# Performance work log

Measured on AMD Instinct MI355X. Metric: run time of the kernel, lower is better.

Reference implementation:

```python
import jax, jax.numpy as jnp
import numpy as np

N, D, H = 24, 256, 8
F = D // H  # 32


def setup_inputs() -> dict:
    key = jax.random.key(0)
    ks = jax.random.split(key, 9)
    T = 8192
    x = jax.random.normal(ks[0], (T, N * D), dtype=jnp.float32)
    s = 0.02
    # Joint-specific query weights: (H, N, D, F); shared K/V: (H, D, F)
    Wq = jax.random.normal(ks[1], (H, N, D, F), dtype=jnp.float32) * s
    bq = jax.random.normal(ks[2], (H, N, F), dtype=jnp.float32) * s
    Wk = jax.random.normal(ks[3], (H, D, F), dtype=jnp.float32) * s
    bk = jax.random.normal(ks[4], (H, F), dtype=jnp.float32) * s
    Wv = jax.random.normal(ks[5], (H, D, F), dtype=jnp.float32) * s
    bv = jax.random.normal(ks[6], (H, F), dtype=jnp.float32) * s
    gamma = jnp.ones((N * D,), dtype=jnp.float32)
    beta = jnp.zeros((N * D,), dtype=jnp.float32)
    return {"x": x, "Wq": Wq, "bq": bq, "Wk": Wk, "bk": bk,
            "Wv": Wv, "bv": bv, "gamma": gamma, "beta": beta}


def reference(x, Wq, bq, Wk, bk, Wv, bv, gamma, beta):
    T = x.shape[0]
    xr = x.reshape(T, N, D)                                   # (T, N, D)
    # Shared K/V per head, joint-specific Q per head
    k = jnp.einsum('tnd,hdf->thnf', xr, Wk) + bk[None, :, None, :]
    v = jnp.einsum('tnd,hdf->thnf', xr, Wv) + bv[None, :, None, :]
    q = jnp.einsum('tnd,hndf->thnf', xr, Wq) + bq[None, :, :, :]
    scores = jnp.einsum('thnf,thmf->thnm', q, k) / jnp.sqrt(jnp.float32(F))
    attn = jax.nn.softmax(scores, axis=-1)                    # (T, H, N, N)
    out = jnp.einsum('thnm,thmf->thnf', attn, v)              # (T, H, N, F)
    # Concat heads -> (T, N, H*F) = (T, N, D)
    out = jnp.transpose(out, (0, 2, 1, 3)).reshape(T, N * D)
    # Dropout is identity in eval mode; residual + LayerNorm over N*D
    y = x + out
    mu = jnp.mean(y, axis=-1, keepdims=True)
    var = jnp.mean((y - mu) ** 2, axis=-1, keepdims=True)
    y = (y - mu) * jax.lax.rsqrt(var + 1e-5)
    return y * gamma + beta
```

## Files before the change

### kernel.cpp

```cpp
#include <hip/hip_runtime.h>

#define NT 8192
#define NJ 24
#define DD 256
#define NH 8
#define FF 32
#define C3 768

typedef __attribute__((ext_vector_type(8))) short bf16x8;
typedef __attribute__((ext_vector_type(4))) float f32x4;

__device__ __forceinline__ unsigned short f2bf(float f) {
    union { float f; unsigned int u; } c; c.f = f;
    unsigned int u = c.u;
    unsigned int r = (u + 0x7fffu + ((u >> 16) & 1u)) >> 16;
    return (unsigned short)r;
}
__device__ __forceinline__ float u2f(unsigned int u) {
    union { unsigned int u; float f; } c; c.u = u;
    return c.f;
}
__device__ __forceinline__ void up8(uint4 w, float* f) {
    f[0] = u2f(w.x << 16); f[1] = u2f(w.x & 0xffff0000u);
    f[2] = u2f(w.y << 16); f[3] = u2f(w.y & 0xffff0000u);
    f[4] = u2f(w.z << 16); f[5] = u2f(w.z & 0xffff0000u);
    f[6] = u2f(w.w << 16); f[7] = u2f(w.w & 0xffff0000u);
}

__device__ __forceinline__ void gload16(const void* g, void* l) {
    __builtin_amdgcn_global_load_lds(
        (const __attribute__((address_space(1))) unsigned int*)g,
        (__attribute__((address_space(3))) unsigned int*)l, 16, 0, 0);
}

__global__ void pack_w(const float* __restrict__ Wq, const float* __restrict__ Wk,
                       const float* __restrict__ Wv, unsigned short* __restrict__ wbt) {
    size_t idx = (size_t)blockIdx.x * 256 + threadIdx.x;
    const size_t total = (size_t)NJ * C3 * DD;
    if (idx >= total) return;
    int d = idx & 255;
    int rest = (int)(idx >> 8);
    int c = rest % C3;
    int n = rest / C3;
    float v;
    if (c < 256) {
        int h = c >> 5, f = c & 31;
        v = Wq[((((size_t)h * NJ + n) * DD) + d) * FF + f];
    } else if (c < 512) {
        int cc = c - 256; int h = cc >> 5, f = cc & 31;
        v = Wk[(((size_t)h * DD) + d) * FF + f];
    } else {
        int cc = c - 512; int h = cc >> 5, f = cc & 31;
        v = Wv[(((size_t)h * DD) + d) * FF + f];
    }
    wbt[idx] = f2bf(v);
}

__global__ void pack_b(const float* __restrict__ bq, const float* __restrict__ bk,
                       const float* __restrict__ bv, float* __restrict__ bias) {
    int idx = blockIdx.x * 256 + threadIdx.x;
    if (idx >= NJ * C3) return;
    int c = idx % C3;
    int n = idx / C3;
    float v;
    if (c < 256) {
        int h = c >> 5, f = c & 31;
        v = bq[((h * NJ + n) * FF) + f];
    } else if (c < 512) {
        int cc = c - 256; int h = cc >> 5, f = cc & 31;
        v = bk[h * FF + f];
    } else {
        int cc = c - 512; int h = cc >> 5, f = cc & 31;
        v = bv[h * FF + f];
    }
    bias[idx] = v;
}

__global__ void pack_x(const float* __restrict__ x, unsigned short* __restrict__ xb) {
    size_t idx = (size_t)blockIdx.x * 256 + threadIdx.x;
    const size_t total = (size_t)NT * NJ * DD / 4;
    if (idx >= total) return;
    float4 v = ((const float4*)x)[idx];
    ushort4 h;
    h.x = f2bf(v.x); h.y = f2bf(v.y); h.z = f2bf(v.z); h.w = f2bf(v.w);
    ((ushort4*)xb)[idx] = h;
}

#define BM 128
#define BN 128

__global__ __launch_bounds__(256, 3)
void gemm_qkv(const unsigned short* __restrict__ xb, const unsigned short* __restrict__ wbt,
              const float* __restrict__ bias, unsigned short* __restrict__ qkv,
              int t0, int mbs) {
    const int nwg = gridDim.x;
    const int cpx = nwg >> 3;
    const int bid = blockIdx.x;
    const int swz = (bid & 7) * cpx + (bid >> 3);
    const int nb = swz % 6;
    const int rest = swz / 6;
    const int mb = rest % mbs;
    const int nj = rest / mbs;

    const int tid = threadIdx.x;
    const int wave = tid >> 6, lane = tid & 63;

    __shared__ unsigned short As[BM * 64];
    __shared__ unsigned short Bs[BN * 64];

    f32x4 acc[4][4];
    #pragma unroll
    for (int i = 0; i < 4; ++i)
        #pragma unroll
        for (int j = 0; j < 4; ++j)
            #pragma unroll
            for (int r = 0; r < 4; ++r) acc[i][j][r] = 0.f;

    const int trow0 = t0 + mb * BM;
    const char* srcA = (const char*)(xb + (size_t)trow0 * (NJ * DD) + nj * DD);
    const char* srcB = (const char*)(wbt + ((size_t)nj * C3 + (size_t)nb * BN) * DD);

    const int rg = lane >> 3;
    const int sc = (lane & 7) ^ rg;

    const int wr = (wave >> 1) * 64;
    const int wc = (wave & 1) * 64;
    const int lr = lane & 15;
    const int g  = lane >> 4;

    for (int kb = 0; kb < 4; ++kb) {
        #pragma unroll
        for (int i = 0; i < 4; ++i) {
            int row0 = wave * 32 + i * 8;
            gload16(srcA + (size_t)(row0 + rg) * (NJ * DD * 2) + kb * 128 + sc * 16,
                    (char*)As + row0 * 128);
        }
        #pragma unroll
        for (int i = 0; i < 4; ++i) {
            int row0 = wave * 32 + i * 8;
            gload16(srcB + (size_t)(row0 + rg) * (DD * 2) + kb * 128 + sc * 16,
                    (char*)Bs + row0 * 128);
        }
        __syncthreads();

        #pragma unroll
        for (int kk = 0; kk < 2; ++kk) {
            bf16x8 a[4], b[4];
            #pragma unroll
            for (int i = 0; i < 4; ++i) {
                int row = wr + i * 16 + lr;
                int c16 = (kk * 4 + g) ^ (row & 7);
                a[i] = *(const bf16x8*)((const char*)As + row * 128 + c16 * 16);
            }
            #pragma unroll
            for (int j = 0; j < 4; ++j) {
                int row = wc + j * 16 + lr;
                int c16 = (kk * 4 + g) ^ (row & 7);
                b[j] = *(const bf16x8*)((const char*)Bs + row * 128 + c16 * 16);
            }
            #pragma unroll
            for (int i = 0; i < 4; ++i)
                #pragma unroll
                for (int j = 0; j < 4; ++j)
                    acc[i][j] = __builtin_amdgcn_mfma_f32_16x16x32_bf16(a[i], b[j], acc[i][j], 0, 0, 0);
        }
        __syncthreads();
    }

    const int ln = lane & 15;
    const int lq = (lane >> 4) * 4;
    float bv[4];
    #pragma unroll
    for (int j = 0; j < 4; ++j)
        bv[j] = bias[nj * C3 + nb * BN + wc + j * 16 + ln];
    #pragma unroll
    for (int i = 0; i < 4; ++i) {
        #pragma unroll
        for (int r = 0; r < 4; ++r) {
            int trow = mb * BM + wr + i * 16 + lq + r;
            size_t base = ((size_t)trow * NJ + nj) * C3 + (size_t)nb * BN;
            #pragma unroll
            for (int j = 0; j < 4; ++j) {
                float val = acc[i][j][r] + bv[j];
                qkv[base + wc + j * 16 + ln] = f2bf(val);
            }
        }
    }
}

__global__ __launch_bounds__(256, 4)
void attn_ln(const unsigned short* __restrict__ qkv, const float* __restrict__ x,
             const float* __restrict__ gamma, const float* __restrict__ beta,
             float* __restrict__ out, int t0) {
    const int tloc = blockIdx.x;
    const int t = t0 + tloc;
    const int tid = threadIdx.x;
    const int wave = tid >> 6, lane = tid & 63;

    __shared__ __align__(16) char smem[NJ * C3 * 2];
    unsigned short* qs = (unsigned short*)smem;
    float* os = (float*)smem;
    __shared__ float red[8];
    __shared__ float stats[2];

    {
        const int4* src = (const int4*)(qkv + (size_t)tloc * NJ * C3);
        int4* dst = (int4*)qs;
        #pragma unroll
        for (int j = 0; j < 9; ++j)
            dst[tid + j * 256] = src[tid + j * 256];
    }
    __syncthreads();

    float o[FF];
    const bool active = tid < NH * NJ;
    int hn = 0, nn = 0;
    if (active) {
        const int h = tid / NJ;
        const int n = tid - h * NJ;
        hn = h; nn = n;
        const int hb = h * FF;
        float qf[FF];
        {
            const uint4* qp = (const uint4*)(qs + n * C3 + hb);
            #pragma unroll
            for (int jj = 0; jj < 4; ++jj) { uint4 w = qp[jj]; up8(w, &qf[jj * 8]); }
        }
        float s[NJ];
        float mx = -1e30f;
        for (int m = 0; m < NJ; ++m) {
            const uint4* kp = (const uint4*)(qs + m * C3 + 256 + hb);
            float a = 0.f;
            #pragma unroll
            for (int jj = 0; jj < 4; ++jj) {
                uint4 w = kp[jj];
                float kf[8]; up8(w, kf);
                #pragma unroll
                for (int e = 0; e < 8; ++e) a += qf[jj * 8 + e] * kf[e];
            }
            a *= 0.17677669529663687f;
            s[m] = a;
            mx = fmaxf(mx, a);
        }
        float sum = 0.f;
        for (int m = 0; m < NJ; ++m) { s[m] = __expf(s[m] - mx); sum += s[m]; }
        float inv = 1.f / sum;
        #pragma unroll
        for (int f = 0; f < FF; ++f) o[f] = 0.f;
        for (int m = 0; m < NJ; ++m) {
            float w = s[m] * inv;
            const uint4* vp = (const uint4*)(qs + m * C3 + 512 + hb);
            #pragma unroll
            for (int jj = 0; jj < 4; ++jj) {
                uint4 wv = vp[jj];
                float vf[8]; up8(wv, vf);
                #pragma unroll
                for (int e = 0; e < 8; ++e) o[jj * 8 + e] += w * vf[e];
            }
        }
    }
    __syncthreads();
    if (active) {
        float* dst = os + nn * DD + hn * FF;
        #pragma unroll
        for (int jj = 0; jj < 8; ++jj)
            *(float4*)(dst + jj * 4) = make_float4(o[jj * 4], o[jj * 4 + 1], o[jj * 4 + 2], o[jj * 4 + 3]);
    }
    __syncthreads();

    const float4* x4 = (const float4*)(x + (size_t)t * (NJ * DD));
    const float4* o4 = (const float4*)os;
    float4 yv[6];
    float sum = 0.f, sq = 0.f;
    #pragma unroll
    for (int j = 0; j < 6; ++j) {
        float4 a = x4[tid + j * 256];
        float4 b = o4[tid + j * 256];
        float4 y;
        y.x = a.x + b.x; y.y = a.y + b.y; y.z = a.z + b.z; y.w = a.w + b.w;
        yv[j] = y;
        sum += y.x + y.y + y.z + y.w;
        sq  += y.x * y.x + y.y * y.y + y.z * y.z + y.w * y.w;
    }
    #pragma unroll
    for (int off = 32; off > 0; off >>= 1) {
        sum += __shfl_down(sum, off);
        sq  += __shfl_down(sq, off);
    }
    if (lane == 0) { red[wave] = sum; red[4 + wave] = sq; }
    __syncthreads();
    if (tid == 0) {
        float s = red[0] + red[1] + red[2] + red[3];
        float q = red[4] + red[5] + red[6] + red[7];
        float mu = s * (1.f / 6144.f);
        float var = q * (1.f / 6144.f) - mu * mu;
        stats[0] = mu;
        stats[1] = rsqrtf(var + 1e-5f);
    }
    __syncthreads();
    const float mu = stats[0], rs = stats[1];
    const float4* g4 = (const float4*)gamma;
    const float4* b4 = (const float4*)beta;
    float4* out4 = (float4*)(out + (size_t)t * (NJ * DD));
    #pragma unroll
    for (int j = 0; j < 6; ++j) {
        float4 g = g4[tid + j * 256];
        float4 bb = b4[tid + j * 256];
        float4 y = yv[j];
        y.x = (y.x - mu) * rs * g.x + bb.x;
        y.y = (y.y - mu) * rs * g.y + bb.y;
        y.z = (y.z - mu) * rs * g.z + bb.z;
        y.w = (y.w - mu) * rs * g.w + bb.w;
        out4[tid + j * 256] = y;
    }
}

extern "C" void kernel_launch(void* const* d_in, const int* in_sizes, int n_in,
                              void* d_out, int out_size, void* d_ws, size_t ws_size,
                              hipStream_t stream) {
    const float* x     = (const float*)d_in[0];
    const float* Wq    = (const float*)d_in[1];
    const float* bq    = (const float*)d_in[2];
    const float* Wk    = (const float*)d_in[3];
    const float* bk    = (const float*)d_in[4];
    const float* Wv    = (const float*)d_in[5];
    const float* bv    = (const float*)d_in[6];
    const float* gamma = (const float*)d_in[7];
    const float* beta  = (const float*)d_in[8];
    float* out = (float*)d_out;

    char* ws = (char*)d_ws;
    const size_t wbt_bytes  = (size_t)NJ * C3 * DD * 2;
    const size_t bias_bytes = (size_t)NJ * C3 * 4;
    const size_t xb_bytes   = (size_t)NT * NJ * DD * 2;
    unsigned short* wbt = (unsigned short*)ws;
    float* bias = (float*)(ws + wbt_bytes);
    unsigned short* xb  = (unsigned short*)(ws + wbt_bytes + bias_bytes);
    unsigned short* qkv = (unsigned short*)(ws + wbt_bytes + bias_bytes + xb_bytes);

    const size_t fixed = wbt_bytes + bias_bytes + xb_bytes;
    size_t avail = (ws_size > fixed) ? ws_size - fixed : 0;
    int chunk = NT;
    while (chunk > BM && (size_t)chunk * NJ * C3 * 2 > avail) chunk >>= 1;

    const size_t wtotal = (size_t)NJ * C3 * DD;
    pack_w<<<dim3((unsigned)((wtotal + 255) / 256)), dim3(256), 0, stream>>>(Wq, Wk, Wv, wbt);
    pack_b<<<dim3((NJ * C3 + 255) / 256), dim3(256), 0, stream>>>(bq, bk, bv, bias);
    const size_t xtotal4 = (size_t)NT * NJ * DD / 4;
    pack_x<<<dim3((unsigned)((xtotal4 + 255) / 256)), dim3(256), 0, stream>>>(x, xb);

    for (int t0 = 0; t0 < NT; t0 += chunk) {
        int mbs = chunk / BM;
        gemm_qkv<<<dim3(6 * mbs * NJ), dim3(256), 0, stream>>>(xb, wbt, bias, qkv, t0, mbs);
        attn_ln<<<dim3(chunk), dim3(256), 0, stream>>>(qkv, x, gamma, beta, out, t0);
    }
}
```

Baseline: 643.4 us.

## Switch QKV to fp16 with packed dot2 attention and slimmer LDS staging

Changes the packed x, weights and QKV intermediate from bf16 to fp16, using the fp16 MFMA in the projection GEMM. In the attention kernel, scores are computed with packed fp16 dot2 instructions and the PV accumulation uses packed half2 FMAs instead of unpacking to fp32. Only K/V are staged in shared memory, with Q read directly from global, and the output tile is XOR-swizzled to reduce LDS bank conflicts. Accumulating the attention output in fp16 reduces precision, and fp16 has a narrower range than bf16.

```diff
diff --git a/kernel.cpp b/kernel.cpp
--- a/kernel.cpp
+++ b/kernel.cpp
@@ -7,24 +7,25 @@
 #define FF 32
 #define C3 768
 
-typedef __attribute__((ext_vector_type(8))) short bf16x8;
+typedef __attribute__((ext_vector_type(8))) _Float16 f16x8;
+typedef __attribute__((ext_vector_type(2))) _Float16 half2v;
 typedef __attribute__((ext_vector_type(4))) float f32x4;
 
-__device__ __forceinline__ unsigned short f2bf(float f) {
-    union { float f; unsigned int u; } c; c.f = f;
-    unsigned int u = c.u;
-    unsigned int r = (u + 0x7fffu + ((u >> 16) & 1u)) >> 16;
-    return (unsigned short)r;
-}
-__device__ __forceinline__ float u2f(unsigned int u) {
-    union { unsigned int u; float f; } c; c.u = u;
-    return c.f;
-}
-__device__ __forceinline__ void up8(uint4 w, float* f) {
-    f[0] = u2f(w.x << 16); f[1] = u2f(w.x & 0xffff0000u);
-    f[2] = u2f(w.y << 16); f[3] = u2f(w.y & 0xffff0000u);
-    f[4] = u2f(w.z << 16); f[5] = u2f(w.z & 0xffff0000u);
-    f[6] = u2f(w.w << 16); f[7] = u2f(w.w & 0xffff0000u);
+__device__ __forceinline__ unsigned short f2h(float f) {
+    union { _Float16 h; unsigned short u; } c;
+    c.h = (_Float16)f;
+    return c.u;
+}
+
+__device__ __forceinline__ float dot2(unsigned int a, unsigned int b, float c) {
+#if __has_builtin(__builtin_amdgcn_fdot2)
+    return __builtin_amdgcn_fdot2(__builtin_bit_cast(half2v, a),
+                                  __builtin_bit_cast(half2v, b), c, false);
+#else
+    half2v ha = __builtin_bit_cast(half2v, a);
+    half2v hb = __builtin_bit_cast(half2v, b);
+    return c + (float)ha[0] * (float)hb[0] + (float)ha[1] * (float)hb[1];
+#endif
 }
 
 __device__ __forceinline__ void gload16(const void* g, void* l) {
@@ -53,7 +54,7 @@
         int cc = c - 512; int h = cc >> 5, f = cc & 31;
         v = Wv[(((size_t)h * DD) + d) * FF + f];
     }
-    wbt[idx] = f2bf(v);
+    wbt[idx] = f2h(v);
 }
 
 __global__ void pack_b(const float* __restrict__ bq, const float* __restrict__ bk,
@@ -82,7 +83,7 @@
     if (idx >= total) return;
     float4 v = ((const float4*)x)[idx];
     ushort4 h;
-    h.x = f2bf(v.x); h.y = f2bf(v.y); h.z = f2bf(v.z); h.w = f2bf(v.w);
+    h.x = f2h(v.x); h.y = f2h(v.y); h.z = f2h(v.z); h.w = f2h(v.w);
     ((ushort4*)xb)[idx] = h;
 }
 
@@ -145,24 +146,24 @@
 
         #pragma unroll
         for (int kk = 0; kk < 2; ++kk) {
-            bf16x8 a[4], b[4];
+            f16x8 a[4], b[4];
             #pragma unroll
             for (int i = 0; i < 4; ++i) {
                 int row = wr + i * 16 + lr;
                 int c16 = (kk * 4 + g) ^ (row & 7);
-                a[i] = *(const bf16x8*)((const char*)As + row * 128 + c16 * 16);
+                a[i] = *(const f16x8*)((const char*)As + row * 128 + c16 * 16);
             }
             #pragma unroll
             for (int j = 0; j < 4; ++j) {
                 int row = wc + j * 16 + lr;
                 int c16 = (kk * 4 + g) ^ (row & 7);
-                b[j] = *(const bf16x8*)((const char*)Bs + row * 128 + c16 * 16);
+                b[j] = *(const f16x8*)((const char*)Bs + row * 128 + c16 * 16);
             }
             #pragma unroll
             for (int i = 0; i < 4; ++i)
                 #pragma unroll
                 for (int j = 0; j < 4; ++j)
-                    acc[i][j] = __builtin_amdgcn_mfma_f32_16x16x32_bf16(a[i], b[j], acc[i][j], 0, 0, 0);
+                    acc[i][j] = __builtin_amdgcn_mfma_f32_16x16x32_f16(a[i], b[j], acc[i][j], 0, 0, 0);
         }
         __syncthreads();
     }
@@ -182,7 +183,7 @@
             #pragma unroll
             for (int j = 0; j < 4; ++j) {
                 float val = acc[i][j][r] + bv[j];
-                qkv[base + wc + j * 16 + ln] = f2bf(val);
+                qkv[base + wc + j * 16 + ln] = f2h(val);
             }
         }
     }
@@ -197,85 +198,99 @@
     const int tid = threadIdx.x;
     const int wave = tid >> 6, lane = tid & 63;
 
-    __shared__ __align__(16) char smem[NJ * C3 * 2];
-    unsigned short* qs = (unsigned short*)smem;
-    float* os = (float*)smem;
+    __shared__ __align__(16) unsigned short kv[NJ * 512];
     __shared__ float red[8];
     __shared__ float stats[2];
-
-    {
-        const int4* src = (const int4*)(qkv + (size_t)tloc * NJ * C3);
-        int4* dst = (int4*)qs;
-        #pragma unroll
-        for (int j = 0; j < 9; ++j)
-            dst[tid + j * 256] = src[tid + j * 256];
-    }
-    __syncthreads();
-
-    float o[FF];
+    float4* os4 = (float4*)kv;
+
+    const uint4* tok = (const uint4*)(qkv + (size_t)tloc * (NJ * C3));
+
+    #pragma unroll
+    for (int j = 0; j < 6; ++j) {
+        int idx = tid + j * 256;
+        int m = idx >> 6, r = idx & 63;
+        ((uint4*)kv)[(m << 6) + r] = tok[m * 96 + 32 + r];
+    }
+
     const bool active = tid < NH * NJ;
-    int hn = 0, nn = 0;
+    const int h = active ? (tid / NJ) : 0;
+    const int n = active ? (tid - h * NJ) : 0;
+    unsigned int qp[16];
     if (active) {
-        const int h = tid / NJ;
-        const int n = tid - h * NJ;
-        hn = h; nn = n;
-        const int hb = h * FF;
-        float qf[FF];
-        {
-            const uint4* qp = (const uint4*)(qs + n * C3 + hb);
-            #pragma unroll
-            for (int jj = 0; jj < 4; ++jj) { uint4 w = qp[jj]; up8(w, &qf[jj * 8]); }
-        }
+        const uint4* qsrc = tok + n * 96 + h * 4;
+        #pragma unroll
+        for (int jj = 0; jj < 4; ++jj) {
+            uint4 w = qsrc[jj];
+            qp[jj * 4 + 0] = w.x; qp[jj * 4 + 1] = w.y;
+            qp[jj * 4 + 2] = w.z; qp[jj * 4 + 3] = w.w;
+        }
+    }
+    __syncthreads();
+
+    half2v o2[16];
+    if (active) {
+        const unsigned short* kbase = kv + h * FF;
         float s[NJ];
         float mx = -1e30f;
+        #pragma unroll
         for (int m = 0; m < NJ; ++m) {
-            const uint4* kp = (const uint4*)(qs + m * C3 + 256 + hb);
+            const uint4* kp = (const uint4*)(kbase + m * 512);
             float a = 0.f;
             #pragma unroll
             for (int jj = 0; jj < 4; ++jj) {
-                uint4 w = kp[jj];
-                float kf[8]; up8(w, kf);
-                #pragma unroll
-                for (int e = 0; e < 8; ++e) a += qf[jj * 8 + e] * kf[e];
+                uint4 kw = kp[jj];
+                a = dot2(kw.x, qp[jj * 4 + 0], a);
+                a = dot2(kw.y, qp[jj * 4 + 1], a);
+                a = dot2(kw.z, qp[jj * 4 + 2], a);
+                a = dot2(kw.w, qp[jj * 4 + 3], a);
             }
             a *= 0.17677669529663687f;
             s[m] = a;
             mx = fmaxf(mx, a);
         }
         float sum = 0.f;
+        #pragma unroll
         for (int m = 0; m < NJ; ++m) { s[m] = __expf(s[m] - mx); sum += s[m]; }
         float inv = 1.f / sum;
         #pragma unroll
-        for (int f = 0; f < FF; ++f) o[f] = 0.f;
+        for (int k = 0; k < 16; ++k) o2[k] = half2v{(_Float16)0.f, (_Float16)0.f};
+        const unsigned short* vbase = kv + 256 + h * FF;
+        #pragma unroll
         for (int m = 0; m < NJ; ++m) {
-            float w = s[m] * inv;
-            const uint4* vp = (const uint4*)(qs + m * C3 + 512 + hb);
+            float wm = s[m] * inv;
+            half2v wv = __builtin_bit_cast(half2v, __builtin_amdgcn_cvt_pkrtz(wm, wm));
+            const uint4* vp = (const uint4*)(vbase + m * 512);
             #pragma unroll
             for (int jj = 0; jj < 4; ++jj) {
-                uint4 wv = vp[jj];
-                float vf[8]; up8(wv, vf);
-                #pragma unroll
-                for (int e = 0; e < 8; ++e) o[jj * 8 + e] += w * vf[e];
+                uint4 vw = vp[jj];
+                o2[jj * 4 + 0] += __builtin_bit_cast(half2v, vw.x) * wv;
+                o2[jj * 4 + 1] += __builtin_bit_cast(half2v, vw.y) * wv;
+                o2[jj * 4 + 2] += __builtin_bit_cast(half2v, vw.z) * wv;
+                o2[jj * 4 + 3] += __builtin_bit_cast(half2v, vw.w) * wv;
             }
         }
     }
     __syncthreads();
     if (active) {
-        float* dst = os + nn * DD + hn * FF;
-        #pragma unroll
-        for (int jj = 0; jj < 8; ++jj)
-            *(float4*)(dst + jj * 4) = make_float4(o[jj * 4], o[jj * 4 + 1], o[jj * 4 + 2], o[jj * 4 + 3]);
+        int base4 = n * 64 + h * 8;
+        #pragma unroll
+        for (int jj = 0; jj < 8; ++jj) {
+            int wi = base4 + jj;
+            int sw = wi ^ ((wi >> 6) & 7);
+            os4[sw] = make_float4((float)o2[jj * 2][0], (float)o2[jj * 2][1],
+                                  (float)o2[jj * 2 + 1][0], (float)o2[jj * 2 + 1][1]);
+        }
     }
     __syncthreads();
 
     const float4* x4 = (const float4*)(x + (size_t)t * (NJ * DD));
-    const float4* o4 = (const float4*)os;
     float4 yv[6];
     float sum = 0.f, sq = 0.f;
     #pragma unroll
     for (int j = 0; j < 6; ++j) {
-        float4 a = x4[tid + j * 256];
-        float4 b = o4[tid + j * 256];
+        int ri = tid + j * 256;
+        float4 a = x4[ri];
+        float4 b = os4[ri ^ ((ri >> 6) & 7)];
         float4 y;
         y.x = a.x + b.x; y.y = a.y + b.y; y.z = a.z + b.z; y.w = a.w + b.w;
         yv[j] = y;
```

After: 620.1 us. 3.6% less time.
